# Optimization experiments

Hardware: AMD Instinct MI355X
Metric: run time of the kernel (lower is better)

## Reference

```python
import jax, jax.numpy as jnp
import numpy as np
from jax import lax

# ---- module constants (match init_kwargs) ----
B, C, H, W = 8, 32, 128, 128
OUT = 32
RB = 1                      # refer_band
GB = (1, 1)                 # init_guard_band
GB_MAX = 3
PAD = GB[0] + RB            # replication pad on all 4 sides (=2)
KH = GB[0] + GB[1] + 2 * RB # kernel_size[0] = 4
KW = 4                      # kernel_size[1]
N = KH * KW                 # 16 ring sampling points
EPS = 1e-5


def _gen_prf():
    """Ring offsets (top,right,bottom,left blocks), matches _gen_prf_grid."""
    rb, gb = RB, GB
    h_prf = (rb + gb[0]) * 2 + 1
    w_prf = (rb + gb[1]) * 2 + 1
    xs = np.arange(-(rb + gb[0]), rb + gb[0] + 1)
    ys = np.arange(-(rb + gb[1]), rb + gb[1] + 1)
    X, Y = np.meshgrid(xs, ys, indexing='ij')
    def ring(A):
        t = A[0:rb, 0:w_prf - rb]
        r = A[0:h_prf - rb, w_prf - rb:w_prf]
        d = A[h_prf - rb:h_prf, rb:w_prf]
        l = A[rb:h_prf, 0:rb]
        return np.concatenate([t.ravel(), r.ravel(), d.ravel(), l.ravel()])
    return ring(X).astype(np.float32), ring(Y).astype(np.float32)

PRF_X, PRF_Y = _gen_prf()  # each (N,)


def _conv(x, w, b, pad, stride=(1, 1)):
    out = lax.conv_general_dilated(
        x, w, stride, [(pad[0], pad[0]), (pad[1], pad[1])],
        dimension_numbers=('NCHW', 'OIHW', 'NCHW'))
    return out + b[None, :, None, None]


def _bn(x, gamma, beta):
    # training-mode batchnorm (biased variance), matching torch default
    m = jnp.mean(x, (0, 2, 3), keepdims=True)
    v = jnp.var(x, (0, 2, 3), keepdims=True)
    return (x - m) * jax.lax.rsqrt(v + EPS) * gamma[None, :, None, None] + beta[None, :, None, None]


def _sample(x_flat, ix, iy, Wp, h, w):
    # x_flat: (B, C, Hp*Wp); ix, iy: (B, h, w, N) int -> (B, C, h, w, N)
    b = ix.shape[0]
    c = x_flat.shape[1]
    idx = (ix * Wp + iy).reshape(b, 1, -1)
    g = jnp.take_along_axis(x_flat, idx, axis=2)
    return g.reshape(b, c, h, w, N)


def _forward(x, w_vrt, b_vrt, g_vrt, be_vrt, w_hrz, b_hrz, g_hrz, be_hrz, w_pk, b_pk):
    b, c, h, w = x.shape
    x_pad = jnp.pad(x, ((0, 0), (0, 0), (PAD, PAD), (PAD, PAD)), mode='edge')
    Hp, Wp = x_pad.shape[2], x_pad.shape[3]
    x_flat = x_pad.reshape(b, c, Hp * Wp)

    # ---- BandEst: per-pixel guard-band widths in 4 directions (B,4,H,W) ----
    v = jax.nn.sigmoid(_bn(_conv(x, w_vrt, b_vrt, (GB_MAX, 0)), g_vrt, be_vrt)) * (GB_MAX - 1)
    hz = jax.nn.sigmoid(_bn(_conv(x, w_hrz, b_hrz, (0, GB_MAX)), g_hrz, be_hrz)) * (GB_MAX - 1)
    gb = jnp.concatenate([v, hz], axis=1)

    # ---- reference-cell sampling positions p = center + ring + learned move ----
    base_x = (jnp.arange(h, dtype=x.dtype) + PAD)[None, :, None, None]
    base_y = (jnp.arange(w, dtype=x.dtype) + PAD)[None, None, :, None]
    p_x = base_x + jnp.asarray(PRF_X)[None, None, None, :]  # (1,H,1,N)->bcast
    p_y = base_y + jnp.asarray(PRF_Y)[None, None, None, :]

    n4 = N // 4  # points per ring side (t,r,d,l ordering)
    def rep(g2):  # (B,H,W) -> (B,H,W,n4)
        return jnp.broadcast_to(g2[..., None], (b, h, w, n4))
    zeros = jnp.zeros((b, h, w, n4), x.dtype)
    move_x = jnp.concatenate([-rep(gb[:, 0]), zeros, rep(gb[:, 1]), zeros], -1)
    move_y = jnp.concatenate([zeros, rep(gb[:, 3]), zeros, -rep(gb[:, 2])], -1)
    p_x = p_x + move_x  # (B,H,W,N)
    p_y = p_y + move_y

    # ---- bilinear (two-corner) gather, mirrors torch q_lt/q_rb/g_lt/g_rb ----
    q_lt_x = jnp.floor(lax.stop_gradient(p_x))
    q_lt_y = jnp.floor(lax.stop_gradient(p_y))
    q_rb_x, q_rb_y = q_lt_x + 1, q_lt_y + 1
    q_lt_xi = jnp.clip(q_lt_x, 0, Hp - 1).astype(jnp.int32)
    q_lt_yi = jnp.clip(q_lt_y, 0, Wp - 1).astype(jnp.int32)
    q_rb_xi = jnp.clip(q_rb_x, 0, Hp - 1).astype(jnp.int32)
    q_rb_yi = jnp.clip(q_rb_y, 0, Wp - 1).astype(jnp.int32)
    p_x = jnp.clip(p_x, 0, Hp - 1)
    p_y = jnp.clip(p_y, 0, Wp - 1)

    g_lt = (1 + (q_lt_xi.astype(p_x.dtype) - p_x)) * (1 + (q_lt_yi.astype(p_y.dtype) - p_y))
    g_rb = (1 - (q_rb_xi.astype(p_x.dtype) - p_x)) * (1 - (q_rb_yi.astype(p_y.dtype) - p_y))

    x_q_lt = _sample(x_flat, q_lt_xi, q_lt_yi, Wp, h, w)  # (B,C,H,W,N)
    x_q_rb = _sample(x_flat, q_rb_xi, q_rb_yi, Wp, h, w)
    x_r = g_lt[:, None] * x_q_lt + g_rb[:, None] * x_q_rb

    # center value x_c equals x itself (center indices land in the interior)
    x_prf = x[:, :, :, :, None] - x_r  # (B,C,H,W,N)

    # ---- _reshape_x_prf: (B,C,H,W,N) -> (B,C,H*KH,W*KW) ----
    xk = x_prf.reshape(b, c, h, w, KH, KW).transpose(0, 1, 2, 4, 3, 5).reshape(b, c, h * KH, w * KW)

    # ---- peak conv: kernel = stride = (KH,KW), no padding ----
    return _conv(xk, w_pk, b_pk, (0, 0), stride=(KH, KW))


def setup_inputs() -> dict:
    key = jax.random.key(0)
    ks = jax.random.split(key, 8)
    s = 0.05
    return {
        'x': jax.random.normal(ks[0], (B, C, H, W), jnp.float32),
        'w_vrt': jax.random.normal(ks[1], (2, C, 2 * GB_MAX + 1, 1), jnp.float32) * s,
        'b_vrt': jax.random.normal(ks[2], (2,), jnp.float32) * s,
        'g_vrt': jnp.ones((2,), jnp.float32),
        'be_vrt': jnp.zeros((2,), jnp.float32),
        'w_hrz': jax.random.normal(ks[3], (2, C, 1, 2 * GB_MAX + 1), jnp.float32) * s,
        'b_hrz': jax.random.normal(ks[4], (2,), jnp.float32) * s,
        'g_hrz': jnp.ones((2,), jnp.float32),
        'be_hrz': jnp.zeros((2,), jnp.float32),
        'w_pk': jax.random.normal(ks[5], (OUT, C, KH, KW), jnp.float32) * s,
        'b_pk': jax.random.normal(ks[6], (OUT,), jnp.float32) * s,
    }


def reference(x, w_vrt, b_vrt, g_vrt, be_vrt, w_hrz, b_hrz, g_hrz, be_hrz, w_pk, b_pk):
    return _forward(x, w_vrt, b_vrt, g_vrt, be_vrt, w_hrz, b_hrz, g_hrz, be_hrz, w_pk, b_pk)
```

## Files before the change

### kernel.cpp

```cpp
#include <hip/hip_runtime.h>
#include <math.h>

#define BB 8
#define CCH 32
#define HH 128
#define WW 128
#define OUTC 32
#define NPIX (BB*HH*WW)
#define HWP 131
#define NCONVBLK 2048

#define WS_XT    0
#define WS_CONV4 (BB*HH*WW*CCH)
#define WS_PART  (WS_CONV4 + BB*HH*WW*4)
#define WS_BNAB  (WS_PART + NCONVBLK*8)
#define WS_WKB   (WS_BNAB + 8)

#define TILE_USH (12*40*5*8)

typedef __attribute__((ext_vector_type(8))) short short8;
typedef __attribute__((ext_vector_type(4))) float f32x4;

__device__ __forceinline__ unsigned short f2bf(float f) {
    unsigned u = __float_as_uint(f);
    unsigned r = (u + 0x7FFFu + ((u >> 16) & 1u)) >> 16;
    return (unsigned short)r;
}
__device__ __forceinline__ unsigned cvtpk(float lo, float hi) {
    unsigned r;
    asm("v_cvt_pk_bf16_f32 %0, %1, %2" : "=v"(r) : "v"(lo), "v"(hi));
    return r;
}
__device__ __forceinline__ float bflo(unsigned w) { return __uint_as_float(w << 16); }
__device__ __forceinline__ float bfhi(unsigned w) { return __uint_as_float(w & 0xFFFF0000u); }

__global__ __launch_bounds__(256) void k_fused1(const float* __restrict__ x,
        const float* __restrict__ w_vrt, const float* __restrict__ b_vrt,
        const float* __restrict__ w_hrz, const float* __restrict__ b_hrz,
        const float* __restrict__ w_pk, float* __restrict__ ws) {
    __shared__ float tile[32][33];
    __shared__ float red[4][64][4];
    int blk = blockIdx.x, t = threadIdx.x;
    if (blk < 4096) {
        int j0 = (blk & 3) << 5;
        int bi = blk >> 2;
        int b = bi >> 7, i = bi & 127;
        int tx = t & 31, ty = t >> 5;
        #pragma unroll
        for (int c = ty; c < 32; c += 8)
            tile[c][tx] = x[(((size_t)b*CCH + c)*HH + i)*WW + j0 + tx];
        __syncthreads();
        float* xt = ws + WS_XT;
        #pragma unroll
        for (int jj = ty; jj < 32; jj += 8)
            xt[(((size_t)bi)*WW + j0 + jj)*CCH + tx] = tile[tx][jj];
    } else if (blk < 4096 + NCONVBLK) {
        int cb = blk - 4096;
        int idx0 = cb * 64;
        int b = idx0 >> 14, ij0 = idx0 & 16383, i = ij0 >> 7, j0c = ij0 & 127;
        int px = t & 63;
        int grp = __builtin_amdgcn_readfirstlane(t >> 6);
        float v0 = 0.f, v1 = 0.f, h0 = 0.f, h1 = 0.f;
        for (int c8 = 0; c8 < 8; c8++) {
            int c = grp * 8 + c8;
            const float* basec = x + ((size_t)(b*CCH + c))*HH*WW;
            #pragma unroll
            for (int k = 0; k < 7; k++) {
                float wv0 = w_vrt[c*7 + k], wv1 = w_vrt[224 + c*7 + k];
                int gr = i + k - 3;
                if (gr >= 0 && gr < HH) {
                    float xv = basec[(size_t)gr*WW + j0c + px];
                    v0 += wv0 * xv; v1 += wv1 * xv;
                }
                float wh0 = w_hrz[c*7 + k], wh1 = w_hrz[224 + c*7 + k];
                int gc = j0c + px + k - 3;
                if (gc >= 0 && gc < WW) {
                    float xh = basec[(size_t)i*WW + gc];
                    h0 += wh0 * xh; h1 += wh1 * xh;
                }
            }
        }
        red[grp][px][0] = v0; red[grp][px][1] = v1;
        red[grp][px][2] = h0; red[grp][px][3] = h1;
        __syncthreads();
        if (grp == 0) {
            float fv0 = red[0][px][0]+red[1][px][0]+red[2][px][0]+red[3][px][0] + b_vrt[0];
            float fv1 = red[0][px][1]+red[1][px][1]+red[2][px][1]+red[3][px][1] + b_vrt[1];
            float fh0 = red[0][px][2]+red[1][px][2]+red[2][px][2]+red[3][px][2] + b_hrz[0];
            float fh1 = red[0][px][3]+red[1][px][3]+red[2][px][3]+red[3][px][3] + b_hrz[1];
            float4* conv4 = (float4*)(ws + WS_CONV4);
            conv4[idx0 + px] = make_float4(fv0, fv1, fh0, fh1);
            float stv[8] = {fv0, fv1, fh0, fh1, fv0*fv0, fv1*fv1, fh0*fh0, fh1*fh1};
            #pragma unroll
            for (int u = 0; u < 8; u++) {
                float s = stv[u];
                for (int off = 32; off; off >>= 1) s += __shfl_down(s, off);
                if (px == 0) ws[WS_PART + cb*8 + u] = s;
            }
        }
    } else {
        unsigned short* wkb = (unsigned short*)(ws + WS_WKB);
        int e = (blk - 4096 - NCONVBLK) * 2048 + t;
        for (int u = 0; u < 8; u++, e += 256) {
            int o = e >> 9, n = (e >> 5) & 15, c = e & 31;
            wkb[o*512 + n*32 + c] = f2bf(w_pk[((o*32 + c) << 4) + n]);
        }
    }
}

__global__ __launch_bounds__(256) void k_prep(
        const float* __restrict__ g_vrt, const float* __restrict__ be_vrt,
        const float* __restrict__ g_hrz, const float* __restrict__ be_hrz,
        float* __restrict__ ws) {
    __shared__ float acc[32][8];
    int t = threadIdx.x;
    int s = t & 7, chunk = t >> 3;
    float sum = 0.f;
    for (int m = 0; m < 64; m++)
        sum += ws[WS_PART + (size_t)(chunk*64 + m)*8 + s];
    acc[chunk][s] = sum;
    __syncthreads();
    if (t < 8) {
        float tot = 0.f;
        #pragma unroll
        for (int c = 0; c < 32; c++) tot += acc[c][t];
        acc[0][t] = tot;
    }
    __syncthreads();
    if (t < 4) {
        const float cnt = (float)NPIX;
        float mean = acc[0][t] / cnt;
        float var  = acc[0][4 + t] / cnt - mean * mean;
        float gamma = (t < 2) ? g_vrt[t] : g_hrz[t - 2];
        float beta  = (t < 2) ? be_vrt[t] : be_hrz[t - 2];
        float a = gamma * rsqrtf(var + 1e-5f);
        ws[WS_BNAB + t]     = a;
        ws[WS_BNAB + 4 + t] = beta - mean * a;
    }
}

__device__ __forceinline__ short8 sample_frag(const unsigned short* tile,
        const float* xc8, const float* gbv, float fi, float fj, int n,
        float prx, float pry, int i0, int j0, int quad) {
    float mx = 0.f, my = 0.f;
    if (n < 4)       mx = -gbv[0];
    else if (n < 8)  my =  gbv[3];
    else if (n < 12) mx =  gbv[1];
    else             my = -gbv[2];
    float px = fi + prx + mx;
    float py = fj + pry + my;
    float qlx = floorf(px), qly = floorf(py);
    int qlxi = min(max((int)qlx, 0), HWP);
    int qlyi = min(max((int)qly, 0), HWP);
    int qrxi = min(max((int)qlx + 1, 0), HWP);
    int qryi = min(max((int)qly + 1, 0), HWP);
    float pxc = fminf(fmaxf(px, 0.f), (float)HWP);
    float pyc = fminf(fmaxf(py, 0.f), (float)HWP);
    float glt = (1.f + ((float)qlxi - pxc)) * (1.f + ((float)qlyi - pyc));
    float grb = (1.f - ((float)qrxi - pxc)) * (1.f - ((float)qryi - pyc));
    float nglt = -glt, ngrb = -grb;
    int ltr = min(max(qlxi - 2, 0), HH - 1), ltc = min(max(qlyi - 2, 0), WW - 1);
    int rbr = min(max(qrxi - 2, 0), HH - 1), rbc = min(max(qryi - 2, 0), WW - 1);
    int lt_off = (ltr - i0 + 4)*1600 + (ltc - j0 + 4)*40 + quad*8;
    int rb_off = (rbr - i0 + 4)*1600 + (rbc - j0 + 4)*40 + quad*8;
    uint4 lw = *(const uint4*)(tile + lt_off);
    uint4 rw = *(const uint4*)(tile + rb_off);
    float d0 = fmaf(nglt, bflo(lw.x), fmaf(ngrb, bflo(rw.x), xc8[0]));
    float d1 = fmaf(nglt, bfhi(lw.x), fmaf(ngrb, bfhi(rw.x), xc8[1]));
    float d2 = fmaf(nglt, bflo(lw.y), fmaf(ngrb, bflo(rw.y), xc8[2]));
    float d3 = fmaf(nglt, bfhi(lw.y), fmaf(ngrb, bfhi(rw.y), xc8[3]));
    float d4 = fmaf(nglt, bflo(lw.z), fmaf(ngrb, bflo(rw.z), xc8[4]));
    float d5 = fmaf(nglt, bfhi(lw.z), fmaf(ngrb, bfhi(rw.z), xc8[5]));
    float d6 = fmaf(nglt, bflo(lw.w), fmaf(ngrb, bflo(rw.w), xc8[6]));
    float d7 = fmaf(nglt, bfhi(lw.w), fmaf(ngrb, bfhi(rw.w), xc8[7]));
    uint4 bw;
    bw.x = cvtpk(d0, d1); bw.y = cvtpk(d2, d3);
    bw.z = cvtpk(d4, d5); bw.w = cvtpk(d6, d7);
    return *(short8*)&bw;
}

__device__ __forceinline__ void frac_setup(float pm, float& ng, int& m) {
    float qf = floorf(pm);
    int qi = min(max((int)qf, 0), HWP);
    float pmc = fminf(fmaxf(pm, 0.f), (float)HWP);
    ng = pmc - (float)qi - 1.f;
    m = min(max(qi - 2, 0), HH - 1);
}
__device__ __forceinline__ short8 samp1(const unsigned short* tile,
        const float* xc8, float ng, int off) {
    uint4 lw = *(const uint4*)(tile + off);
    float d0 = fmaf(ng, bflo(lw.x), xc8[0]);
    float d1 = fmaf(ng, bfhi(lw.x), xc8[1]);
    float d2 = fmaf(ng, bflo(lw.y), xc8[2]);
    float d3 = fmaf(ng, bfhi(lw.y), xc8[3]);
    float d4 = fmaf(ng, bflo(lw.z), xc8[4]);
    float d5 = fmaf(ng, bfhi(lw.z), xc8[5]);
    float d6 = fmaf(ng, bflo(lw.w), xc8[6]);
    float d7 = fmaf(ng, bfhi(lw.w), xc8[7]);
    uint4 bw;
    bw.x = cvtpk(d0, d1); bw.y = cvtpk(d2, d3);
    bw.z = cvtpk(d4, d5); bw.w = cvtpk(d6, d7);
    return *(short8*)&bw;
}

__global__ __launch_bounds__(256, 4) void k_main(const float* __restrict__ ws,
        const float* __restrict__ b_pk, float* __restrict__ out) {
    __shared__ unsigned short tile[TILE_USH];
    const float* xt   = ws + WS_XT;
    const float* bnab = ws + WS_BNAB;
    const unsigned short* wkb = (const unsigned short*)(ws + WS_WKB);
    const float prfx[16] = {-2,-2,-2,-2, -2,-1, 0, 1,  2, 2, 2, 2, -1, 0, 1, 2};
    const float prfy[16] = {-2,-1, 0, 1,  2, 2, 2, 2, -1, 0, 1, 2, -2,-2,-2,-2};
    const int ioffs[16]  = {-2,-1, 0, 1, -2,-1, 0, 1, -1, 0, 1, 2, -1, 0, 1, 2};

    int t = threadIdx.x;
    int blk = blockIdx.x;
    int b = blk >> 7;
    int i0 = ((blk >> 2) & 31) * 4;
    int j0 = (blk & 3) * 32;

    for (int s = t; s < 12*40*4; s += 256) {
        int q = s & 3, cc = (s >> 2) % 40, r = (s >> 2) / 40;
        int gr = min(max(i0 - 4 + r, 0), HH - 1);
        int gc = min(max(j0 - 4 + cc, 0), WW - 1);
        const float4* src = (const float4*)(xt + (((size_t)(b*HH + gr))*WW + gc)*CCH + q*8);
        float4 f0 = src[0], f1 = src[1];
        uint4 v;
        v.x = cvtpk(f0.x, f0.y); v.y = cvtpk(f0.z, f0.w);
        v.z = cvtpk(f1.x, f1.y); v.w = cvtpk(f1.z, f1.w);
        *(uint4*)(tile + ((r*40 + cc)*5 + q)*8) = v;
    }
    __syncthreads();

    int w = t >> 6, pl = t & 15, quad = (t >> 4) & 3;
    int ir = i0 + w;
    int pjA = j0 + pl, pjB = j0 + 16 + pl;
    int pixA = (b << 14) + ir * WW + pjA;
    int pixB = pixA + 16;
    int q8 = quad * 8;

    float xcA[8], xcB[8];
    {
        const float4* xpA = (const float4*)(xt + (size_t)pixA * CCH + q8);
        float4 v0 = xpA[0], v1 = xpA[1];
        xcA[0]=v0.x; xcA[1]=v0.y; xcA[2]=v0.z; xcA[3]=v0.w;
        xcA[4]=v1.x; xcA[5]=v1.y; xcA[6]=v1.z; xcA[7]=v1.w;
        const float4* xpB = (const float4*)(xt + (size_t)pixB * CCH + q8);
        float4 u0 = xpB[0], u1 = xpB[1];
        xcB[0]=u0.x; xcB[1]=u0.y; xcB[2]=u0.z; xcB[3]=u0.w;
        xcB[4]=u1.x; xcB[5]=u1.y; xcB[6]=u1.z; xcB[7]=u1.w;
    }
    const float4* conv4 = (const float4*)(ws + WS_CONV4);
    float4 cvA = conv4[pixA], cvB = conv4[pixB];
    float gbvA[4], gbvB[4];
    gbvA[0] = 2.f / (1.f + expf(-(cvA.x * bnab[0] + bnab[4])));
    gbvA[1] = 2.f / (1.f + expf(-(cvA.y * bnab[1] + bnab[5])));
    gbvA[2] = 2.f / (1.f + expf(-(cvA.z * bnab[2] + bnab[6])));
    gbvA[3] = 2.f / (1.f + expf(-(cvA.w * bnab[3] + bnab[7])));
    gbvB[0] = 2.f / (1.f + expf(-(cvB.x * bnab[0] + bnab[4])));
    gbvB[1] = 2.f / (1.f + expf(-(cvB.y * bnab[1] + bnab[5])));
    gbvB[2] = 2.f / (1.f + expf(-(cvB.z * bnab[2] + bnab[6])));
    gbvB[3] = 2.f / (1.f + expf(-(cvB.w * bnab[3] + bnab[7])));

    f32x4 accA0 = {0.f,0.f,0.f,0.f}, accA1 = {0.f,0.f,0.f,0.f};
    f32x4 accB0 = {0.f,0.f,0.f,0.f}, accB1 = {0.f,0.f,0.f,0.f};
    float fi = (float)ir + 2.f;
    float fjA = (float)pjA + 2.f, fjB = (float)pjB + 2.f;

    short8 a0 = *(const short8*)(wkb + (size_t)pl * 512 + q8);
    short8 a1 = *(const short8*)(wkb + (size_t)(pl + 16) * 512 + q8);

    float ngA_ = 0.f, ngB_ = 0.f;
    int baseA_ = 0, baseB_ = 0;

    #pragma unroll
    for (int n = 0; n < 16; n++) {
        short8 na0 = a0, na1 = a1;
        if (n < 15) {
            na0 = *(const short8*)(wkb + (size_t)pl * 512 + (n+1)*32 + q8);
            na1 = *(const short8*)(wkb + (size_t)(pl + 16) * 512 + (n+1)*32 + q8);
        }
        if ((n & 3) == 0) {
            int g = n >> 2;
            float pmA, pmB;
            if (g == 0)      { pmA = (fi  - 2.f) - gbvA[0]; pmB = (fi  - 2.f) - gbvB[0]; }
            else if (g == 1) { pmA = (fjA + 2.f) + gbvA[3]; pmB = (fjB + 2.f) + gbvB[3]; }
            else if (g == 2) { pmA = (fi  + 2.f) + gbvA[1]; pmB = (fi  + 2.f) + gbvB[1]; }
            else             { pmA = (fjA - 2.f) - gbvA[2]; pmB = (fjB - 2.f) - gbvB[2]; }
            int mA, mB;
            frac_setup(pmA, ngA_, mA);
            frac_setup(pmB, ngB_, mB);
            if ((g & 1) == 0) {
                baseA_ = (mA - i0 + 4)*1600 + q8;
                baseB_ = (mB - i0 + 4)*1600 + q8;
            } else {
                baseA_ = (mA - j0 + 4)*40 + q8;
                baseB_ = (mB - j0 + 4)*40 + q8;
            }
        }
        short8 bfA, bfB;
        if (n == 11 || n == 15) {
            bfA = sample_frag(tile, xcA, gbvA, fi, fjA, n, prfx[n], prfy[n], i0, j0, quad);
            bfB = sample_frag(tile, xcB, gbvB, fi, fjB, n, prfx[n], prfy[n], i0, j0, quad);
        } else {
            int io = ioffs[n];
            int offA, offB;
            if (((n >> 2) & 1) == 0) {
                int cA = min(max(pjA + io, 0), WW - 1);
                int cB = min(max(pjB + io, 0), WW - 1);
                offA = baseA_ + (cA - j0 + 4)*40;
                offB = baseB_ + (cB - j0 + 4)*40;
            } else {
                int r  = min(max(ir + io, 0), HH - 1);
                int rt = (r - i0 + 4)*1600;
                offA = baseA_ + rt;
                offB = baseB_ + rt;
            }
            bfA = samp1(tile, xcA, ngA_, offA);
            bfB = samp1(tile, xcB, ngB_, offB);
        }
        accA0 = __builtin_amdgcn_mfma_f32_16x16x32_bf16(a0, bfA, accA0, 0, 0, 0);
        accA1 = __builtin_amdgcn_mfma_f32_16x16x32_bf16(a1, bfA, accA1, 0, 0, 0);
        accB0 = __builtin_amdgcn_mfma_f32_16x16x32_bf16(a0, bfB, accB0, 0, 0, 0);
        accB1 = __builtin_amdgcn_mfma_f32_16x16x32_bf16(a1, bfB, accB1, 0, 0, 0);
        a0 = na0; a1 = na1;
    }
    float* opA = out + (size_t)b * (OUTC*HH*WW) + ir * WW + pjA;
    float* opB = opA + 16;
    #pragma unroll
    for (int r = 0; r < 4; r++) {
        int o = quad*4 + r;
        float bo = b_pk[o], bo16 = b_pk[o + 16];
        opA[(size_t)o * (HH*WW)]        = accA0[r] + bo;
        opA[(size_t)(o + 16) * (HH*WW)] = accA1[r] + bo16;
        opB[(size_t)o * (HH*WW)]        = accB0[r] + bo;
        opB[(size_t)(o + 16) * (HH*WW)] = accB1[r] + bo16;
    }
}

extern "C" void kernel_launch(void* const* d_in, const int* in_sizes, int n_in,
                              void* d_out, int out_size, void* d_ws, size_t ws_size,
                              hipStream_t stream) {
    const float* x      = (const float*)d_in[0];
    const float* w_vrt  = (const float*)d_in[1];
    const float* b_vrt  = (const float*)d_in[2];
    const float* g_vrt  = (const float*)d_in[3];
    const float* be_vrt = (const float*)d_in[4];
    const float* w_hrz  = (const float*)d_in[5];
    const float* b_hrz  = (const float*)d_in[6];
    const float* g_hrz  = (const float*)d_in[7];
    const float* be_hrz = (const float*)d_in[8];
    const float* w_pk   = (const float*)d_in[9];
    const float* b_pk   = (const float*)d_in[10];
    float* ws  = (float*)d_ws;
    float* out = (float*)d_out;

    k_fused1<<<4096 + NCONVBLK + 8, 256, 0, stream>>>(x, w_vrt, b_vrt, w_hrz, b_hrz, w_pk, ws);
    k_prep<<<1, 256, 0, stream>>>(g_vrt, be_vrt, g_hrz, be_hrz, ws);
    k_main<<<1024, 256, 0, stream>>>(ws, b_pk, out);
}
```

Before: 151.0 us.

## Store transposed input as bf16, fuse BN stat reduction into main kernel

Measured after the change: 150.9 us. No clear change (-0.1%).

```diff
diff --git a/kernel.cpp b/kernel.cpp
--- a/kernel.cpp
+++ b/kernel.cpp
@@ -10,11 +10,10 @@
 #define HWP 131
 #define NCONVBLK 2048
 
-#define WS_XT    0
-#define WS_CONV4 (BB*HH*WW*CCH)
+#define WS_XTB   0
+#define WS_CONV4 (BB*HH*WW*CCH/2)
 #define WS_PART  (WS_CONV4 + BB*HH*WW*4)
-#define WS_BNAB  (WS_PART + NCONVBLK*8)
-#define WS_WKB   (WS_BNAB + 8)
+#define WS_WKB   (WS_PART + NCONVBLK*8)
 
 #define TILE_USH (12*40*5*8)
 
@@ -50,10 +49,14 @@
         for (int c = ty; c < 32; c += 8)
             tile[c][tx] = x[(((size_t)b*CCH + c)*HH + i)*WW + j0 + tx];
         __syncthreads();
-        float* xt = ws + WS_XT;
+        unsigned* xtb4 = (unsigned*)(ws + WS_XTB);
+        int cp = t & 15, jy = t >> 4;
         #pragma unroll
-        for (int jj = ty; jj < 32; jj += 8)
-            xt[(((size_t)bi)*WW + j0 + jj)*CCH + tx] = tile[tx][jj];
+        for (int u = 0; u < 2; u++) {
+            int jj = jy + u*16;
+            unsigned v = cvtpk(tile[2*cp][jj], tile[2*cp + 1][jj]);
+            xtb4[((size_t)bi*WW + j0 + jj)*16 + cp] = v;
+        }
     } else if (blk < 4096 + NCONVBLK) {
         int cb = blk - 4096;
         int idx0 = cb * 64;
@@ -105,37 +108,6 @@
             int o = e >> 9, n = (e >> 5) & 15, c = e & 31;
             wkb[o*512 + n*32 + c] = f2bf(w_pk[((o*32 + c) << 4) + n]);
         }
-    }
-}
-
-__global__ __launch_bounds__(256) void k_prep(
-        const float* __restrict__ g_vrt, const float* __restrict__ be_vrt,
-        const float* __restrict__ g_hrz, const float* __restrict__ be_hrz,
-        float* __restrict__ ws) {
-    __shared__ float acc[32][8];
-    int t = threadIdx.x;
-    int s = t & 7, chunk = t >> 3;
-    float sum = 0.f;
-    for (int m = 0; m < 64; m++)
-        sum += ws[WS_PART + (size_t)(chunk*64 + m)*8 + s];
-    acc[chunk][s] = sum;
-    __syncthreads();
-    if (t < 8) {
-        float tot = 0.f;
-        #pragma unroll
-        for (int c = 0; c < 32; c++) tot += acc[c][t];
-        acc[0][t] = tot;
-    }
-    __syncthreads();
-    if (t < 4) {
-        const float cnt = (float)NPIX;
-        float mean = acc[0][t] / cnt;
-        float var  = acc[0][4 + t] / cnt - mean * mean;
-        float gamma = (t < 2) ? g_vrt[t] : g_hrz[t - 2];
-        float beta  = (t < 2) ? be_vrt[t] : be_hrz[t - 2];
-        float a = gamma * rsqrtf(var + 1e-5f);
-        ws[WS_BNAB + t]     = a;
-        ws[WS_BNAB + 4 + t] = beta - mean * a;
     }
 }
 
@@ -204,17 +176,22 @@
 }
 
 __global__ __launch_bounds__(256, 4) void k_main(const float* __restrict__ ws,
+        const float* __restrict__ x,
+        const float* __restrict__ g_vrt, const float* __restrict__ be_vrt,
+        const float* __restrict__ g_hrz, const float* __restrict__ be_hrz,
         const float* __restrict__ b_pk, float* __restrict__ out) {
     __shared__ unsigned short tile[TILE_USH];
-    const float* xt   = ws + WS_XT;
-    const float* bnab = ws + WS_BNAB;
+    __shared__ float racc[32][8];
+    __shared__ float bnab_s[8];
+    const unsigned short* xtb = (const unsigned short*)(ws + WS_XTB);
     const unsigned short* wkb = (const unsigned short*)(ws + WS_WKB);
+    const float* part = ws + WS_PART;
     const float prfx[16] = {-2,-2,-2,-2, -2,-1, 0, 1,  2, 2, 2, 2, -1, 0, 1, 2};
     const float prfy[16] = {-2,-1, 0, 1,  2, 2, 2, 2, -1, 0, 1, 2, -2,-2,-2,-2};
     const int ioffs[16]  = {-2,-1, 0, 1, -2,-1, 0, 1, -1, 0, 1, 2, -1, 0, 1, 2};
 
     int t = threadIdx.x;
-    int blk = blockIdx.x;
+    int blk = ((blockIdx.x & 7) << 7) | (blockIdx.x >> 3);
     int b = blk >> 7;
     int i0 = ((blk >> 2) & 31) * 4;
     int j0 = (blk & 3) * 32;
@@ -223,12 +200,34 @@
         int q = s & 3, cc = (s >> 2) % 40, r = (s >> 2) / 40;
         int gr = min(max(i0 - 4 + r, 0), HH - 1);
         int gc = min(max(j0 - 4 + cc, 0), WW - 1);
-        const float4* src = (const float4*)(xt + (((size_t)(b*HH + gr))*WW + gc)*CCH + q*8);
-        float4 f0 = src[0], f1 = src[1];
-        uint4 v;
-        v.x = cvtpk(f0.x, f0.y); v.y = cvtpk(f0.z, f0.w);
-        v.z = cvtpk(f1.x, f1.y); v.w = cvtpk(f1.z, f1.w);
+        uint4 v = *(const uint4*)(xtb + (((size_t)(b*HH + gr))*WW + gc)*CCH + q*8);
         *(uint4*)(tile + ((r*40 + cc)*5 + q)*8) = v;
+    }
+    {
+        int s8 = t & 7, chunk = t >> 3;
+        float sum = 0.f;
+        #pragma unroll 8
+        for (int m = 0; m < 64; m++)
+            sum += part[(size_t)(chunk*64 + m)*8 + s8];
+        racc[chunk][s8] = sum;
+    }
+    __syncthreads();
+    if (t < 8) {
+        float tot = 0.f;
+        #pragma unroll
+        for (int c = 0; c < 32; c++) tot += racc[c][t];
+        racc[0][t] = tot;
+    }
+    __syncthreads();
+    if (t < 4) {
+        const float cnt = (float)NPIX;
+        float mean = racc[0][t] / cnt;
+        float var  = racc[0][4 + t] / cnt - mean * mean;
+        float gamma = (t < 2) ? g_vrt[t] : g_hrz[t - 2];
+        float beta  = (t < 2) ? be_vrt[t] : be_hrz[t - 2];
+        float a = gamma * rsqrtf(var + 1e-5f);
+        bnab_s[t]     = a;
+        bnab_s[4 + t] = beta - mean * a;
     }
     __syncthreads();
 
@@ -241,26 +240,25 @@
 
     float xcA[8], xcB[8];
     {
-        const float4* xpA = (const float4*)(xt + (size_t)pixA * CCH + q8);
-        float4 v0 = xpA[0], v1 = xpA[1];
-        xcA[0]=v0.x; xcA[1]=v0.y; xcA[2]=v0.z; xcA[3]=v0.w;
-        xcA[4]=v1.x; xcA[5]=v1.y; xcA[6]=v1.z; xcA[7]=v1.w;
-        const float4* xpB = (const float4*)(xt + (size_t)pixB * CCH + q8);
-        float4 u0 = xpB[0], u1 = xpB[1];
-        xcB[0]=u0.x; xcB[1]=u0.y; xcB[2]=u0.z; xcB[3]=u0.w;
-        xcB[4]=u1.x; xcB[5]=u1.y; xcB[6]=u1.z; xcB[7]=u1.w;
+        const float* xb = x + (size_t)b * CCH * HH * WW + (size_t)ir * WW;
+        #pragma unroll
+        for (int k = 0; k < 8; k++) {
+            const float* p = xb + (size_t)(q8 + k) * (HH * WW);
+            xcA[k] = p[pjA];
+            xcB[k] = p[pjB];
+        }
     }
     const float4* conv4 = (const float4*)(ws + WS_CONV4);
     float4 cvA = conv4[pixA], cvB = conv4[pixB];
     float gbvA[4], gbvB[4];
-    gbvA[0] = 2.f / (1.f + expf(-(cvA.x * bnab[0] + bnab[4])));
-    gbvA[1] = 2.f / (1.f + expf(-(cvA.y * bnab[1] + bnab[5])));
-    gbvA[2] = 2.f / (1.f + expf(-(cvA.z * bnab[2] + bnab[6])));
-    gbvA[3] = 2.f / (1.f + expf(-(cvA.w * bnab[3] + bnab[7])));
-    gbvB[0] = 2.f / (1.f + expf(-(cvB.x * bnab[0] + bnab[4])));
-    gbvB[1] = 2.f / (1.f + expf(-(cvB.y * bnab[1] + bnab[5])));
-    gbvB[2] = 2.f / (1.f + expf(-(cvB.z * bnab[2] + bnab[6])));
-    gbvB[3] = 2.f / (1.f + expf(-(cvB.w * bnab[3] + bnab[7])));
+    gbvA[0] = 2.f / (1.f + expf(-(cvA.x * bnab_s[0] + bnab_s[4])));
+    gbvA[1] = 2.f / (1.f + expf(-(cvA.y * bnab_s[1] + bnab_s[5])));
+    gbvA[2] = 2.f / (1.f + expf(-(cvA.z * bnab_s[2] + bnab_s[6])));
+    gbvA[3] = 2.f / (1.f + expf(-(cvA.w * bnab_s[3] + bnab_s[7])));
+    gbvB[0] = 2.f / (1.f + expf(-(cvB.x * bnab_s[0] + bnab_s[4])));
+    gbvB[1] = 2.f / (1.f + expf(-(cvB.y * bnab_s[1] + bnab_s[5])));
+    gbvB[2] = 2.f / (1.f + expf(-(cvB.z * bnab_s[2] + bnab_s[6])));
+    gbvB[3] = 2.f / (1.f + expf(-(cvB.w * bnab_s[3] + bnab_s[7])));
 
     f32x4 accA0 = {0.f,0.f,0.f,0.f}, accA1 = {0.f,0.f,0.f,0.f};
     f32x4 accB0 = {0.f,0.f,0.f,0.f}, accB1 = {0.f,0.f,0.f,0.f};
@@ -356,6 +354,5 @@
     float* out = (float*)d_out;
 
     k_fused1<<<4096 + NCONVBLK + 8, 256, 0, stream>>>(x, w_vrt, b_vrt, w_hrz, b_hrz, w_pk, ws);
-    k_prep<<<1, 256, 0, stream>>>(g_vrt, be_vrt, g_hrz, be_hrz, ws);
-    k_main<<<1024, 256, 0, stream>>>(ws, b_pk, out);
-}
+    k_main<<<1024, 256, 0, stream>>>(ws, x, g_vrt, be_vrt, g_hrz, be_hrz, b_pk, out);
+}
```
